# Kernel optimization log

Measured on AMD Instinct MI355X. Metric: run time of the kernel, lower is better.

Reference implementation:

```python
import jax, jax.numpy as jnp
import numpy as np

HEADS = 16


def setup_inputs() -> dict:
    key = jax.random.key(0)
    k1, k2, k3, k4, k5, k6 = jax.random.split(key, 6)
    L, B, H = 1024, 8, 2048
    dk = H // HEADS
    std = 1.0 / np.sqrt(H)
    return {
        "query": jax.random.normal(k1, (B, H), dtype=jnp.float32),
        "feed_hiddens": jax.random.normal(k2, (L, B, H), dtype=jnp.float32),
        "values": jax.random.normal(k3, (L, B, H), dtype=jnp.float32),
        # additive-attention params (reconstructed from forward's shape constraints)
        "attn_w": jax.random.normal(k4, (2 * dk, H), dtype=jnp.float32) * std,
        "bias": jax.random.normal(k5, (H,), dtype=jnp.float32) * std,
        "score": jax.random.normal(k6, (H, 1), dtype=jnp.float32) * std,
    }


def reference(query, feed_hiddens, values, attn_w, bias, score):
    L, B, H = feed_hiddens.shape
    dk = H // HEADS
    # q: [B, h, 1, dk]; k, v: [B, h, L, dk]
    q = query.reshape(B, HEADS, 1, dk)
    k = feed_hiddens.reshape(L, B, HEADS, dk).transpose(1, 2, 0, 3)
    v = values.reshape(L, B, HEADS, dk).transpose(1, 2, 0, 3)
    # cat([q_rep, k], -1) @ attn_w  ==  q @ Wq + k @ Wk  (avoids the repeat/concat blowup)
    Wq, Wk = attn_w[:dk], attn_w[dk:]
    energy = jax.nn.relu(q @ Wq + k @ Wk + bias)        # [B, h, L, H]
    logits = (energy @ score).transpose(0, 1, 3, 2)     # [B, h, 1, L]
    a = jax.nn.softmax(logits, axis=-1)
    out = (a @ v).reshape(B, H)[None]                   # [1, B, H]
    return out
```

## Files before the change

kernel.cpp:

```cpp
#include <hip/hip_runtime.h>
#include <hip/hip_bf16.h>
#include <hip/hip_fp8.h>

#define HEADS 16
#define B_    8
#define H_    2048
#define L_    1024
#define DK    128

typedef __attribute__((ext_vector_type(8))) int   i32x8;
typedef __attribute__((ext_vector_type(4))) int   i32x4;
typedef __attribute__((ext_vector_type(4))) float f32x4;

__device__ __forceinline__ unsigned u8e4m3(float x) {
  __hip_fp8_e4m3 f8(x);
  return (unsigned)f8.__x;
}

__device__ __forceinline__ void gload_lds16(const void* g, void* l) {
  __builtin_amdgcn_global_load_lds(
      (const __attribute__((address_space(1))) void*)g,
      (__attribute__((address_space(3))) void*)l, 16, 0, 0);
}

__global__ void __launch_bounds__(256)
prep_kernel(const float* __restrict__ query,
            const float* __restrict__ attn_w,
            const float* __restrict__ bias,
            const float* __restrict__ score,
            float2* __restrict__ qs2,
            unsigned char* __restrict__ wk8) {
  const int tid = threadIdx.x;
  if (blockIdx.x < 128) {
    const int jt = blockIdx.x & 7;
    const int bg = blockIdx.x >> 3;
    __shared__ float qv[8][DK];
    for (int i = tid; i < 8 * DK; i += 256) {
      const int bh = bg * 8 + (i >> 7);
      const int d  = i & 127;
      const int b = bh >> 4, head = bh & 15;
      qv[i >> 7][d] = query[b * H_ + head * DK + d];
    }
    __syncthreads();
    const int j = jt * 256 + tid;
    const float bj = bias[j];
    const float sj = score[j] * (1.0f / 64.0f);
    float acc[8];
#pragma unroll
    for (int u = 0; u < 8; ++u) acc[u] = bj;
    for (int d = 0; d < DK; ++d) {
      const float wv = attn_w[d * H_ + j];
#pragma unroll
      for (int u = 0; u < 8; ++u) acc[u] += qv[u][d] * wv;
    }
#pragma unroll
    for (int u = 0; u < 8; ++u) {
      float2 t; t.x = 64.0f * acc[u]; t.y = sj;
      qs2[(size_t)(bg * 8 + u) * H_ + j] = t;
    }
  } else {
    const int t0 = (blockIdx.x - 128) * 256 + tid;
    for (int tt = t0; tt < 8192; tt += 4096) {
      const int l  = tt & 63;
      const int nc = tt >> 6;
      const int n  = nc * 16 + (l & 15);
      const int k0 = (l >> 4) * 32;
#pragma unroll
      for (int half = 0; half < 2; ++half) {
        unsigned w[4];
#pragma unroll
        for (int j = 0; j < 4; ++j) {
          unsigned v = 0;
#pragma unroll
          for (int byt = 0; byt < 4; ++byt) {
            const int i = half * 16 + j * 4 + byt;
            const float x = 64.0f * attn_w[(size_t)(DK + k0 + i) * H_ + n];
            v |= u8e4m3(x) << (8 * byt);
          }
          w[j] = v;
        }
        uint4 q; q.x = w[0]; q.y = w[1]; q.z = w[2]; q.w = w[3];
        *(uint4*)(wk8 + (size_t)nc * 2048 + half * 1024 + l * 16) = q;
      }
    }
  }
}

__global__ void __launch_bounds__(256, 2)
logits_kernel(const float* __restrict__ feed,
              const unsigned char* __restrict__ wk8,
              const float2* __restrict__ qs2,
              float* __restrict__ logits) {
  const int ltile = blockIdx.x;
  const int bh    = blockIdx.y;
  const int b     = bh >> 4;
  const int head  = bh & 15;
  const int tid   = threadIdx.x;
  const int wave  = tid >> 6;
  const int lane  = tid & 63;
  const int row   = lane & 15;
  const int g     = lane >> 4;

  __shared__ unsigned char ring[4][8192];
  __shared__ float2 qs[H_];

#pragma unroll
  for (int u = 0; u < 8; ++u)
    qs[tid + 256 * u] = qs2[(size_t)bh * H_ + tid + 256 * u];

  i32x8 aF[4];
#pragma unroll
  for (int s = 0; s < 4; ++s) {
    const int l = ltile * 256 + wave * 64 + s * 16 + row;
    const float* fh = feed + (size_t)l * (B_ * H_) + b * H_ + head * DK + g * 32;
    i32x8 af;
#pragma unroll
    for (int j = 0; j < 8; ++j) {
      float4 x = *(const float4*)(fh + j * 4);
      unsigned v = u8e4m3(x.x) | (u8e4m3(x.y) << 8) |
                   (u8e4m3(x.z) << 16) | (u8e4m3(x.w) << 24);
      af[j] = (int)v;
    }
    aF[s] = af;
  }
  __syncthreads();

  const char* wkb   = (const char*)wk8;
  char*       ringb = (char*)ring;

#pragma unroll
  for (int ph = 0; ph < 2; ++ph) {
#pragma unroll
    for (int i = 0; i < 2; ++i)
      gload_lds16(wkb + (size_t)ph * 8192 + wave * 2048 + i * 1024 + lane * 16,
                  ringb + ph * 8192 + wave * 2048 + i * 1024);
  }

  float lacc[4][4] = {};

#pragma unroll 1
  for (int p = 0; p < 32; ++p) {
    const int pf = (p + 2 < 32) ? p + 2 : 31;
    const int ws = ((p + 2) & 3) * 8192;
    gload_lds16(wkb + (size_t)pf * 8192 + wave * 2048 + 0    + lane * 16,
                ringb + ws + wave * 2048 + 0);
    gload_lds16(wkb + (size_t)pf * 8192 + wave * 2048 + 1024 + lane * 16,
                ringb + ws + wave * 2048 + 1024);

    __builtin_amdgcn_sched_barrier(0);
    asm volatile("s_waitcnt vmcnt(4)" ::: "memory");
    __builtin_amdgcn_s_barrier();
    __builtin_amdgcn_sched_barrier(0);

    const char* rs = ringb + (p & 3) * 8192;
#pragma unroll
    for (int cc = 0; cc < 4; ++cc) {
      const char* rc = rs + cc * 2048 + lane * 16;
      i32x4 lo = *(const i32x4*)(rc);
      i32x4 hi = *(const i32x4*)(rc + 1024);
      i32x8 b8;
      b8[0] = lo[0]; b8[1] = lo[1]; b8[2] = lo[2]; b8[3] = lo[3];
      b8[4] = hi[0]; b8[5] = hi[1]; b8[6] = hi[2]; b8[7] = hi[3];
      const float2 q2 = qs[(4 * p + cc) * 16 + row];
      const float qx = q2.x, qy = q2.y;

      f32x4 d0 = {qx, qx, qx, qx};
      f32x4 d1 = {qx, qx, qx, qx};
      f32x4 d2 = {qx, qx, qx, qx};
      f32x4 d3 = {qx, qx, qx, qx};
      d0 = __builtin_amdgcn_mfma_scale_f32_16x16x128_f8f6f4(
             aF[0], b8, d0, 0, 0, 0, 0x7F7F7F7F, 0, 0x7F7F7F7F);
      d1 = __builtin_amdgcn_mfma_scale_f32_16x16x128_f8f6f4(
             aF[1], b8, d1, 0, 0, 0, 0x7F7F7F7F, 0, 0x7F7F7F7F);
      d2 = __builtin_amdgcn_mfma_scale_f32_16x16x128_f8f6f4(
             aF[2], b8, d2, 0, 0, 0, 0x7F7F7F7F, 0, 0x7F7F7F7F);
      d3 = __builtin_amdgcn_mfma_scale_f32_16x16x128_f8f6f4(
             aF[3], b8, d3, 0, 0, 0, 0x7F7F7F7F, 0, 0x7F7F7F7F);

#pragma unroll
      for (int i = 0; i < 4; ++i) {
        lacc[0][i] += fmaxf(d0[i], 0.f) * qy;
        lacc[1][i] += fmaxf(d1[i], 0.f) * qy;
        lacc[2][i] += fmaxf(d2[i], 0.f) * qy;
        lacc[3][i] += fmaxf(d3[i], 0.f) * qy;
      }
    }
  }

#pragma unroll
  for (int s = 0; s < 4; ++s) {
#pragma unroll
    for (int i = 0; i < 4; ++i) {
      float v = lacc[s][i];
#pragma unroll
      for (int off = 1; off < 16; off <<= 1) v += __shfl_xor(v, off);
      lacc[s][i] = v;
    }
  }
  if (row == 0) {
#pragma unroll
    for (int s = 0; s < 4; ++s) {
      const int base = bh * L_ + ltile * 256 + wave * 64 + s * 16 + g * 4;
#pragma unroll
      for (int i = 0; i < 4; ++i) logits[base + i] = lacc[s][i];
    }
  }
}

__global__ void __launch_bounds__(256)
softmax_pv_kernel(const float* __restrict__ logits,
                  const float* __restrict__ values,
                  float* __restrict__ out) {
  const int bh    = blockIdx.x;
  const int dpart = blockIdx.y;
  const int b     = bh >> 4;
  const int head  = bh & 15;
  const int tid   = threadIdx.x;

  __shared__ float  sl[L_];
  __shared__ float  sred[4];
  __shared__ float  sscal;
  __shared__ float4 pacc[32][8];

  float m = -1e30f;
  for (int i = tid; i < L_; i += 256) {
    float v = logits[(size_t)bh * L_ + i];
    sl[i] = v;
    m = fmaxf(m, v);
  }
#pragma unroll
  for (int off = 32; off > 0; off >>= 1) m = fmaxf(m, __shfl_xor(m, off));
  if ((tid & 63) == 0) sred[tid >> 6] = m;
  __syncthreads();
  if (tid == 0) {
    float mm = fmaxf(fmaxf(sred[0], sred[1]), fmaxf(sred[2], sred[3]));
    sscal = mm;
  }
  __syncthreads();
  const float mx = sscal;

  float s = 0.f;
  for (int i = tid; i < L_; i += 256) {
    float e = __expf(sl[i] - mx);
    sl[i] = e;
    s += e;
  }
#pragma unroll
  for (int off = 32; off > 0; off >>= 1) s += __shfl_xor(s, off);
  if ((tid & 63) == 0) sred[tid >> 6] = s;
  __syncthreads();
  if (tid == 0) {
    sscal = 1.0f / ((sred[0] + sred[1]) + (sred[2] + sred[3]));
  }
  __syncthreads();
  const float inv = sscal;

  const int dq4  = tid & 7;
  const int lsub = tid >> 3;
  const float4* vp = (const float4*)(values + (size_t)b * H_ + head * DK + dpart * 32) + dq4;
  float4 acc = {0.f, 0.f, 0.f, 0.f};
  for (int ll = lsub; ll < L_; ll += 32) {
    const float w = sl[ll];
    float4 v = vp[(size_t)ll * (B_ * H_ / 4)];
    acc.x += w * v.x; acc.y += w * v.y; acc.z += w * v.z; acc.w += w * v.w;
  }
  pacc[lsub][dq4] = acc;
  __syncthreads();
  if (tid < 64) {
    const int q = tid & 7, k = tid >> 3;
    float4 a0 = pacc[k][q], a1 = pacc[k + 8][q], a2 = pacc[k + 16][q], a3 = pacc[k + 24][q];
    float4 r;
    r.x = (a0.x + a1.x) + (a2.x + a3.x);
    r.y = (a0.y + a1.y) + (a2.y + a3.y);
    r.z = (a0.z + a1.z) + (a2.z + a3.z);
    r.w = (a0.w + a1.w) + (a2.w + a3.w);
    pacc[k][q] = r;
  }
  __syncthreads();
  if (tid < 8) {
    float4 t = {0.f, 0.f, 0.f, 0.f};
#pragma unroll
    for (int k = 0; k < 8; ++k) {
      float4 a = pacc[k][tid];
      t.x += a.x; t.y += a.y; t.z += a.z; t.w += a.w;
    }
    t.x *= inv; t.y *= inv; t.z *= inv; t.w *= inv;
    *(float4*)(out + (size_t)b * H_ + head * DK + dpart * 32 + tid * 4) = t;
  }
}

extern "C" void kernel_launch(void* const* d_in, const int* in_sizes, int n_in,
                              void* d_out, int out_size, void* d_ws, size_t ws_size,
                              hipStream_t stream) {
  const float* query  = (const float*)d_in[0];
  const float* feed   = (const float*)d_in[1];
  const float* values = (const float*)d_in[2];
  const float* attn_w = (const float*)d_in[3];
  const float* bias   = (const float*)d_in[4];
  const float* score  = (const float*)d_in[5];
  float* out = (float*)d_out;

  float2*        qs2    = (float2*)d_ws;
  unsigned char* wk8    = (unsigned char*)d_ws + (size_t)(B_ * HEADS * H_) * sizeof(float2);
  float*         logits = (float*)(wk8 + (size_t)H_ * DK);

  prep_kernel<<<144, 256, 0, stream>>>(query, attn_w, bias, score, qs2, wk8);
  logits_kernel<<<dim3(L_ / 256, B_ * HEADS), 256, 0, stream>>>(feed, wk8, qs2, logits);
  softmax_pv_kernel<<<dim3(B_ * HEADS, 4), 256, 0, stream>>>(logits, values, out);
}
```

Baseline: 84.28 us.

## Split logits kernel over two N-halves and pack q/score as bf16 pairs

The logits kernel grid gains a z-dimension of 2. Each block handles half of the 2048 hidden columns, and the two partial logit sums are added in the softmax kernel. The per-bh query-projection/score table is packed into one 32-bit word of two bf16 values, which halves its LDS footprint and global traffic. This doubles the block count from 512 to 1024 for better occupancy and load balance on the GPU. In exchange, every block re-reads and re-quantizes the feed tile, and bf16 lowers the precision of the qx/qy terms.

```diff
diff --git a/kernel.cpp b/kernel.cpp
--- a/kernel.cpp
+++ b/kernel.cpp
@@ -28,7 +28,7 @@
             const float* __restrict__ attn_w,
             const float* __restrict__ bias,
             const float* __restrict__ score,
-            float2* __restrict__ qs2,
+            unsigned* __restrict__ qsp,
             unsigned char* __restrict__ wk8) {
   const int tid = threadIdx.x;
   if (blockIdx.x < 128) {
@@ -44,7 +44,8 @@
     __syncthreads();
     const int j = jt * 256 + tid;
     const float bj = bias[j];
-    const float sj = score[j] * (1.0f / 64.0f);
+    const unsigned short us =
+        __builtin_bit_cast(unsigned short, (__bf16)(score[j] * (1.0f / 64.0f)));
     float acc[8];
 #pragma unroll
     for (int u = 0; u < 8; ++u) acc[u] = bj;
@@ -55,8 +56,9 @@
     }
 #pragma unroll
     for (int u = 0; u < 8; ++u) {
-      float2 t; t.x = 64.0f * acc[u]; t.y = sj;
-      qs2[(size_t)(bg * 8 + u) * H_ + j] = t;
+      const unsigned short uq =
+          __builtin_bit_cast(unsigned short, (__bf16)(64.0f * acc[u]));
+      qsp[(size_t)(bg * 8 + u) * H_ + j] = ((unsigned)uq << 16) | us;
     }
   } else {
     const int t0 = (blockIdx.x - 128) * 256 + tid;
@@ -89,10 +91,11 @@
 __global__ void __launch_bounds__(256, 2)
 logits_kernel(const float* __restrict__ feed,
               const unsigned char* __restrict__ wk8,
-              const float2* __restrict__ qs2,
+              const unsigned* __restrict__ qsp,
               float* __restrict__ logits) {
   const int ltile = blockIdx.x;
   const int bh    = blockIdx.y;
+  const int nblk  = blockIdx.z;
   const int b     = bh >> 4;
   const int head  = bh & 15;
   const int tid   = threadIdx.x;
@@ -102,11 +105,11 @@
   const int g     = lane >> 4;
 
   __shared__ unsigned char ring[4][8192];
-  __shared__ float2 qs[H_];
-
-#pragma unroll
-  for (int u = 0; u < 8; ++u)
-    qs[tid + 256 * u] = qs2[(size_t)bh * H_ + tid + 256 * u];
+  __shared__ unsigned qsl[1024];
+
+#pragma unroll
+  for (int u = 0; u < 4; ++u)
+    qsl[tid + 256 * u] = qsp[(size_t)bh * H_ + nblk * 1024 + tid + 256 * u];
 
   i32x8 aF[4];
 #pragma unroll
@@ -125,7 +128,7 @@
   }
   __syncthreads();
 
-  const char* wkb   = (const char*)wk8;
+  const char* wkb   = (const char*)wk8 + (size_t)nblk * 131072;
   char*       ringb = (char*)ring;
 
 #pragma unroll
@@ -139,8 +142,8 @@
   float lacc[4][4] = {};
 
 #pragma unroll 1
-  for (int p = 0; p < 32; ++p) {
-    const int pf = (p + 2 < 32) ? p + 2 : 31;
+  for (int p = 0; p < 16; ++p) {
+    const int pf = (p + 2 < 16) ? p + 2 : 15;
     const int ws = ((p + 2) & 3) * 8192;
     gload_lds16(wkb + (size_t)pf * 8192 + wave * 2048 + 0    + lane * 16,
                 ringb + ws + wave * 2048 + 0);
@@ -161,8 +164,9 @@
       i32x8 b8;
       b8[0] = lo[0]; b8[1] = lo[1]; b8[2] = lo[2]; b8[3] = lo[3];
       b8[4] = hi[0]; b8[5] = hi[1]; b8[6] = hi[2]; b8[7] = hi[3];
-      const float2 q2 = qs[(4 * p + cc) * 16 + row];
-      const float qx = q2.x, qy = q2.y;
+      const unsigned qu = qsl[(4 * p + cc) * 16 + row];
+      const float qx = __uint_as_float(qu & 0xffff0000u);
+      const float qy = __uint_as_float(qu << 16);
 
       f32x4 d0 = {qx, qx, qx, qx};
       f32x4 d1 = {qx, qx, qx, qx};
@@ -198,11 +202,12 @@
     }
   }
   if (row == 0) {
+    float* lout = logits + (size_t)nblk * (128 * L_);
 #pragma unroll
     for (int s = 0; s < 4; ++s) {
       const int base = bh * L_ + ltile * 256 + wave * 64 + s * 16 + g * 4;
 #pragma unroll
-      for (int i = 0; i < 4; ++i) logits[base + i] = lacc[s][i];
+      for (int i = 0; i < 4; ++i) lout[base + i] = lacc[s][i];
     }
   }
 }
@@ -224,7 +229,8 @@
 
   float m = -1e30f;
   for (int i = tid; i < L_; i += 256) {
-    float v = logits[(size_t)bh * L_ + i];
+    float v = logits[(size_t)bh * L_ + i] +
+              logits[(size_t)(128 * L_) + bh * L_ + i];
     sl[i] = v;
     m = fmaxf(m, v);
   }
@@ -300,11 +306,11 @@
   const float* score  = (const float*)d_in[5];
   float* out = (float*)d_out;
 
-  float2*        qs2    = (float2*)d_ws;
-  unsigned char* wk8    = (unsigned char*)d_ws + (size_t)(B_ * HEADS * H_) * sizeof(float2);
+  unsigned*      qsp    = (unsigned*)d_ws;
+  unsigned char* wk8    = (unsigned char*)d_ws + (size_t)(B_ * HEADS * H_) * sizeof(unsigned);
   float*         logits = (float*)(wk8 + (size_t)H_ * DK);
 
-  prep_kernel<<<144, 256, 0, stream>>>(query, attn_w, bias, score, qs2, wk8);
-  logits_kernel<<<dim3(L_ / 256, B_ * HEADS), 256, 0, stream>>>(feed, wk8, qs2, logits);
+  prep_kernel<<<144, 256, 0, stream>>>(query, attn_w, bias, score, qsp, wk8);
+  logits_kernel<<<dim3(L_ / 256, B_ * HEADS, 2), 256, 0, stream>>>(feed, wk8, qsp, logits);
   softmax_pv_kernel<<<dim3(B_ * HEADS, 4), 256, 0, stream>>>(logits, values, out);
 }
```

Measured after the change: 85.63 us. Within noise of the previous version (+1.6%).
